# Performance work log

Measured on AMD Instinct MI355X. Metric: run time of the kernel, lower is better.

The kernel has to match this reference:

```python
import jax, jax.numpy as jnp
import numpy as np

B, N, D, K = 4, 8192, 128, 16


def setup_inputs() -> dict:
    key = jax.random.key(0)
    ks = jax.random.split(key, 12)
    w = lambda k, s: (jax.random.normal(k, s, jnp.float32) * 0.02)
    return {
        "xyz": jax.random.normal(ks[0], (B, N, 3), jnp.float32),
        "feat": jax.random.normal(ks[1], (B, N, D), jnp.float32),
        # Linear weights stored as (in, out); apply as x @ W + b
        "Wq": w(ks[2], (D, D)), "bq": jnp.zeros((D,), jnp.float32),
        "Wk": w(ks[3], (D, D)), "bk": jnp.zeros((D,), jnp.float32),
        "Wv": w(ks[4], (D, D)), "bv": jnp.zeros((D,), jnp.float32),
        "Wp1": w(ks[5], (3, D)), "bp1": jnp.zeros((D,), jnp.float32),
        "Wp2": w(ks[6], (D, D)), "bp2": jnp.zeros((D,), jnp.float32),
        "Wo": w(ks[7], (D, D)), "bo": jnp.zeros((D,), jnp.float32),
        "gamma": jnp.float32(0.5),
    }


def reference(xyz, feat, Wq, bq, Wk, bk, Wv, bv, Wp1, bp1, Wp2, bp2, Wo, bo, gamma):
    # pairwise squared distance (B,N,N)
    sq = jnp.sum(xyz * xyz, axis=-1)
    dist = sq[:, :, None] + sq[:, None, :] - 2.0 * jnp.einsum("bnc,bmc->bnm", xyz, xyz)
    # K nearest neighbors (smallest distance)
    _, idx = jax.lax.top_k(-dist, K)  # (B,N,K)
    bidx = jnp.arange(B)[:, None, None]
    n_xyz = xyz[bidx, idx]    # (B,N,K,3)
    n_feat = feat[bidx, idx]  # (B,N,K,D)

    q = (feat @ Wq + bq)[:, :, None, :]    # (B,N,1,D)
    kk = n_feat @ Wk + bk                  # (B,N,K,D)
    v = n_feat @ Wv + bv                   # (B,N,K,D)

    rel_pos = xyz[:, :, None, :] - n_xyz   # (B,N,K,3)
    pos_enc = jax.nn.relu(rel_pos @ Wp1 + bp1) @ Wp2 + bp2  # (B,N,K,D)

    # per-channel-summed attention score, softmax over neighbor axis
    score = jnp.sum(q - kk + pos_enc, axis=-1, keepdims=True)  # (B,N,K,1)
    attn = jax.nn.softmax(score, axis=-2)

    agg = jnp.sum(attn * (v + pos_enc), axis=2)  # (B,N,D)
    out = agg @ Wo + bo
    return feat + gamma * out
```

## Files before the change

kernel.cpp:

```cpp
#include <hip/hip_runtime.h>
#include <hip/hip_bf16.h>

#define BATCH 4
#define NPTS  8192
#define DIM   128
#define KNN   16
#define NROWS (BATCH * NPTS)

#define SPLITS 16
#define RANGE  512
#define TILE   256
#define DEPTH  32
#define DEPTHP 33
#define NSUB   8

using u64  = unsigned long long;
using u32  = unsigned int;

__device__ __forceinline__ unsigned short f2bf(float f) {
    u32 u = __float_as_uint(f);
    u32 r = (u + 0x7FFFu + ((u >> 16) & 1u)) >> 16;
    return (unsigned short)r;
}
__device__ __forceinline__ u32 fordkey(float f) {
    u32 u = __float_as_uint(f);
    return (u & 0x80000000u) ? ~u : (u | 0x80000000u);
}
__device__ __forceinline__ float invkey(u32 k) {
    u32 u = (k & 0x80000000u) ? (k & 0x7FFFFFFFu) : ~k;
    return __uint_as_float(u);
}

__device__ __forceinline__ void insert16u(u32 key, u32* ks) {
    if (key < ks[15]) {
#pragma unroll
        for (int t = 0; t < 16; ++t) {
            u32 lo = key < ks[t] ? key : ks[t];
            u32 hi = key < ks[t] ? ks[t] : key;
            ks[t] = lo;
            key = hi;
        }
    }
}

__device__ __forceinline__ float pdist(float4 me, float4 c) {
    float dot = __fadd_rn(__fadd_rn(__fmul_rn(me.x, c.x), __fmul_rn(me.y, c.y)),
                          __fmul_rn(me.z, c.z));
    return __fsub_rn(__fadd_rn(me.w, c.w), __fmul_rn(2.0f, dot));
}

__global__ __launch_bounds__(256) void prep_weights(const float* __restrict__ Wk,
                                                    const float* __restrict__ Wp2,
                                                    float* __restrict__ wk,
                                                    float* __restrict__ w2) {
    int tid = threadIdx.x;
    int c = tid & 127;
    const float* src = (tid < 128) ? Wk : Wp2;
    float s = 0.f;
    for (int d = 0; d < DIM; ++d) s += src[c * DIM + d];
    if (tid < 128) wk[c] = s;
    else           w2[c] = s;
}

__global__ __launch_bounds__(256) void conv_weights(const float* __restrict__ Wv,
                                                    const float* __restrict__ Wp2,
                                                    const float* __restrict__ Wo,
                                                    u32* __restrict__ Wb) {
    int i = blockIdx.x * 256 + threadIdx.x;
    int which = i >> 13, off = i & 8191;
    const float* W = (which == 0) ? Wv : (which == 1 ? Wp2 : Wo);
    float2 w = ((const float2*)W)[off];
    Wb[i] = (u32)f2bf(w.x) | ((u32)f2bf(w.y) << 16);
}

__global__ __launch_bounds__(256) void prep_points(const float* __restrict__ xyz,
                                                   const float* __restrict__ feat,
                                                   const float* __restrict__ wk,
                                                   float4* __restrict__ pts,
                                                   float* __restrict__ sK) {
    int lid = threadIdx.x & 63;
    int p = blockIdx.x * 4 + (threadIdx.x >> 6);
    float f_lo = feat[(size_t)p * DIM + lid];
    float f_hi = feat[(size_t)p * DIM + 64 + lid];
    float s = fmaf(f_lo, wk[lid], f_hi * wk[64 + lid]);
#pragma unroll
    for (int m = 32; m >= 1; m >>= 1) s += __shfl_xor(s, m);
    if (lid == 0) {
        float x = xyz[p * 3 + 0];
        float y = xyz[p * 3 + 1];
        float z = xyz[p * 3 + 2];
        float sq = __fadd_rn(__fadd_rn(__fmul_rn(x, x), __fmul_rn(y, y)), __fmul_rn(z, z));
        pts[p] = make_float4(x, y, z, sq);
        sK[p] = s;
    }
}

__global__ __launch_bounds__(256) void knn_limpass(const float4* __restrict__ pts,
                                                   float* __restrict__ dlim) {
    __shared__ float4 tile[256];
    int y = blockIdx.y;
    int wavein = threadIdx.x >> 6, lane = threadIdx.x & 63;
    int q = blockIdx.x * 256 + wavein * 64 + lane;
    int b = q >> 13;
    float4 me = pts[q];
    {
        float4 c = pts[b * NPTS + y * 256 + threadIdx.x];
        tile[threadIdx.x] = make_float4(c.x, c.y, c.z, -0.5f * c.w);
    }
    __syncthreads();
    float ks[16];
#pragma unroll
    for (int t = 0; t < 16; ++t) ks[t] = INFINITY;

    for (int jj = 0; jj < 32; ++jj) {
        float4 c = tile[jj];
        float s = fmaf(me.x, c.x, fmaf(me.y, c.y, fmaf(me.z, c.z, c.w)));
        float d = fmaf(-2.0f, s, me.w);
        if (d < ks[15]) {
#pragma unroll
            for (int t = 0; t < 16; ++t) {
                float lo = fminf(d, ks[t]);
                float hi = fmaxf(d, ks[t]);
                ks[t] = lo;
                d = hi;
            }
        }
    }
    float lim = ks[15];
    float A = 0.5f * (me.w - lim);
    for (int c0 = 32; c0 < 256; c0 += 32) {
        u32 mask = 0;
#pragma unroll
        for (int jj = 0; jj < 32; ++jj) {
            float4 c = tile[c0 + jj];
            float s = fmaf(me.x, c.x, fmaf(me.y, c.y, fmaf(me.z, c.z, c.w)));
            mask = (mask << 1) | (u32)(s >= A);
        }
        while (mask) {
            int pos = __builtin_ctz(mask);
            mask &= mask - 1;
            int jj = c0 + 31 - pos;
            float4 c = tile[jj];
            float s = fmaf(me.x, c.x, fmaf(me.y, c.y, fmaf(me.z, c.z, c.w)));
            float d = fmaf(-2.0f, s, me.w);
            if (d < ks[15]) {
#pragma unroll
                for (int t = 0; t < 16; ++t) {
                    float lo = fminf(d, ks[t]);
                    float hi = fmaxf(d, ks[t]);
                    ks[t] = lo;
                    d = hi;
                }
            }
        }
        lim = ks[15];
        A = 0.5f * (me.w - lim);
    }
    dlim[(size_t)y * NROWS + q] = ks[15];
}

__global__ __launch_bounds__(256) void knn_partial(const float4* __restrict__ pts,
                                                   const float* __restrict__ dlim,
                                                   unsigned short* __restrict__ part16) {
    __shared__ float4 tile[TILE];
    __shared__ unsigned char stk[4][64][DEPTHP];
    int r = blockIdx.y;
    int wavein = threadIdx.x >> 6, lane = threadIdx.x & 63;
    int q = blockIdx.x * 256 + wavein * 64 + lane;
    int b = q >> 13;
    float4 me = pts[q];

    float T = dlim[q];
#pragma unroll
    for (int y = 1; y < NSUB; ++y) T = fminf(T, dlim[(size_t)y * NROWS + q]);
    float gate_d = T + 2.0e-4f;
    u32 kk[16];
#pragma unroll
    for (int t = 0; t < 16; ++t) kk[t] = 0xFFFFFFFFu;
    float A = 0.5f * (me.w - gate_d) - 1.0e-4f;
    unsigned char* mystk = stk[wavein][lane];

    for (int tb = 0; tb < RANGE / TILE; ++tb) {
        __syncthreads();
        int jb = r * RANGE + tb * TILE;
        {
            float4 c = pts[b * NPTS + jb + threadIdx.x];
            tile[threadIdx.x] = make_float4(c.x, c.y, c.z, -0.5f * c.w);
        }
        __syncthreads();

        int cnt = 0;
#pragma unroll 4
        for (int jj = 0; jj < TILE; ++jj) {
            float4 c = tile[jj];
            float s = fmaf(me.x, c.x, fmaf(me.y, c.y, fmaf(me.z, c.z, c.w)));
            int slot = cnt < (DEPTH - 1) ? cnt : (DEPTH - 1);
            mystk[slot] = (unsigned char)jj;
            cnt += (s >= A) ? 1 : 0;
        }
        bool over = (cnt >= DEPTH);
        int dn = over ? 0 : cnt;
        for (int i = 0; i < dn; ++i) {
            int jj = mystk[i];
            float4 c = tile[jj];
            float s = fmaf(me.x, c.x, fmaf(me.y, c.y, fmaf(me.z, c.z, c.w)));
            float dt = fmaf(-2.0f, s, me.w);
            u32 key = (fordkey(dt) & 0xFFFFE000u) | (u32)(jb + jj);
            insert16u(key, kk);
        }
        if (__any(over)) {
            if (over) {
                for (int jj = 0; jj < TILE; ++jj) {
                    float4 c = tile[jj];
                    float s = fmaf(me.x, c.x, fmaf(me.y, c.y, fmaf(me.z, c.z, c.w)));
                    if (s >= A) {
                        float dt = fmaf(-2.0f, s, me.w);
                        u32 key = (fordkey(dt) & 0xFFFFE000u) | (u32)(jb + jj);
                        insert16u(key, kk);
                    }
                }
            }
        }
        float nl = invkey((kk[15] & 0xFFFFE000u) | 0x1FFFu) + 1.0e-4f;
        gate_d = (nl < gate_d) ? nl : gate_d;
        A = 0.5f * (me.w - gate_d) - 1.0e-4f;
    }
    u32* dst = (u32*)(part16 + (size_t)q * 256 + r * 16);
#pragma unroll
    for (int t = 0; t < 8; ++t) {
        u32 a = kk[2 * t], c = kk[2 * t + 1];
        u32 i0 = (a == 0xFFFFFFFFu) ? 0xFFFFu : (a & 0x1FFFu);
        u32 i1 = (c == 0xFFFFFFFFu) ? 0xFFFFu : (c & 0x1FFFu);
        dst[t] = i0 | (i1 << 16);
    }
}

__global__ __launch_bounds__(256) void knn_merge(const float4* __restrict__ pts,
                                                 const unsigned short* __restrict__ part16,
                                                 int* __restrict__ idx16) {
    int wavein = threadIdx.x >> 6, lane = threadIdx.x & 63;
    int q = blockIdx.x * 4 + wavein;
    int b = q >> 13;
    float4 me = pts[q];
    ushort4 e = *(const ushort4*)(part16 + (size_t)q * 256 + lane * 4);
    u64 k0, k1, k2, k3;
    {
        u32 id;
        id = e.x; k0 = (id != 0xFFFFu) ? (((u64)fordkey(pdist(me, pts[b * NPTS + id])) << 32) | id) : ~0ull;
        id = e.y; k1 = (id != 0xFFFFu) ? (((u64)fordkey(pdist(me, pts[b * NPTS + id])) << 32) | id) : ~0ull;
        id = e.z; k2 = (id != 0xFFFFu) ? (((u64)fordkey(pdist(me, pts[b * NPTS + id])) << 32) | id) : ~0ull;
        id = e.w; k3 = (id != 0xFFFFu) ? (((u64)fordkey(pdist(me, pts[b * NPTS + id])) << 32) | id) : ~0ull;
    }
    u64 t;
    if (k1 < k0) { t = k0; k0 = k1; k1 = t; }
    if (k3 < k2) { t = k2; k2 = k3; k3 = t; }
    if (k2 < k0) { t = k0; k0 = k2; k2 = t; }
    if (k3 < k1) { t = k1; k1 = k3; k3 = t; }
    if (k2 < k1) { t = k1; k1 = k2; k2 = t; }

    u64 cur = k0;
    int head = 0;
    u64 got = 0;
#pragma unroll
    for (int it = 0; it < 16; ++it) {
        u64 m = cur;
#pragma unroll
        for (int s = 32; s >= 1; s >>= 1) {
            u64 o = __shfl_xor(m, s);
            m = (o < m) ? o : m;
        }
        if (m == cur) {
            head++;
            cur = (head == 1) ? k1 : (head == 2) ? k2 : (head == 3) ? k3 : ~0ull;
        }
        if (lane == it) got = m;
    }
    if (lane < 16) idx16[q * KNN + lane] = (int)(got & 0xFFFFFFFFu);
}

template <int MODE>
__global__ __launch_bounds__(256) void gemm32(const float* __restrict__ X,
                                              const u32* __restrict__ Wb,
                                              const float* __restrict__ bias,
                                              const float* __restrict__ add,
                                              const float* __restrict__ featb,
                                              const float* __restrict__ gammap,
                                              float* __restrict__ outv) {
    __shared__ u32 Ws[DIM * DIM / 2];
    __shared__ float Xs[8 * DIM];
    __shared__ float bs[DIM];
    int tid = threadIdx.x;
    {
        const uint4* src = (const uint4*)Wb;
        uint4* dst = (uint4*)Ws;
        for (int i = tid; i < DIM * DIM / 8; i += 256) dst[i] = src[i];
    }
    if (tid < 128) bs[tid] = bias[tid];
    float gamma = 0.f;
    if (MODE == 2) gamma = *gammap;

    int rowBase = blockIdx.x * 32;
    int d4 = (tid & 31) * 4;
    int row = tid >> 5;

    for (int it = 0; it < 4; ++it) {
        int r0 = rowBase + it * 8;
        __syncthreads();
        ((float4*)Xs)[tid] = ((const float4*)(X + (size_t)r0 * DIM))[tid];
        __syncthreads();

        float a0 = bs[d4], a1 = bs[d4 + 1], a2 = bs[d4 + 2], a3 = bs[d4 + 3];
        const float* xr = &Xs[row * DIM];
#pragma unroll 8
        for (int c = 0; c < DIM; ++c) {
            float x = xr[c];
            uint2 w = *(const uint2*)&Ws[c * (DIM / 2) + (d4 >> 1)];
            a0 = fmaf(x, __uint_as_float(w.x << 16), a0);
            a1 = fmaf(x, __uint_as_float(w.x & 0xFFFF0000u), a1);
            a2 = fmaf(x, __uint_as_float(w.y << 16), a2);
            a3 = fmaf(x, __uint_as_float(w.y & 0xFFFF0000u), a3);
        }
        size_t off = (size_t)(r0 + row) * DIM + d4;
        if (MODE == 1) {
            float4 ad = *(const float4*)(add + off);
            a0 += ad.x; a1 += ad.y; a2 += ad.z; a3 += ad.w;
        }
        if (MODE == 2) {
            float4 fb = *(const float4*)(featb + off);
            a0 = fmaf(gamma, a0, fb.x);
            a1 = fmaf(gamma, a1, fb.y);
            a2 = fmaf(gamma, a2, fb.z);
            a3 = fmaf(gamma, a3, fb.w);
        }
        *(float4*)(outv + off) = make_float4(a0, a1, a2, a3);
    }
}

__global__ __launch_bounds__(256) void stage_c(const float4* __restrict__ pts,
                                               const int* __restrict__ idx16,
                                               const float* __restrict__ sK,
                                               const float* __restrict__ w2,
                                               const float* __restrict__ Wp1,
                                               const float* __restrict__ bp1,
                                               const float* __restrict__ Vf,
                                               float* __restrict__ vagg,
                                               float* __restrict__ hbar) {
    __shared__ float hs[4][KNN * DIM];
    int wavein = threadIdx.x >> 6;
    int lid = threadIdx.x & 63;
    int p = blockIdx.x * 4 + wavein;
    int b = p >> 13;
    float4 me = pts[p];

    float wx_lo = Wp1[lid],        wx_hi = Wp1[64 + lid];
    float wy_lo = Wp1[128 + lid],  wy_hi = Wp1[192 + lid];
    float wz_lo = Wp1[256 + lid],  wz_hi = Wp1[320 + lid];
    float bl    = bp1[lid],        bh    = bp1[64 + lid];
    float w2l   = w2[lid],         w2h   = w2[64 + lid];

    int myidx = idx16[p * KNN + (lid & 15)];
    float* h = hs[wavein];
    float sc = -INFINITY;

    for (int k = 0; k < KNN; ++k) {
        int j = __shfl(myidx, k);
        int g = b * NPTS + j;
        float4 nb = pts[g];
        float rx = me.x - nb.x, ry = me.y - nb.y, rz = me.z - nb.z;
        float h_lo = fmaxf(0.f, fmaf(rx, wx_lo, fmaf(ry, wy_lo, fmaf(rz, wz_lo, bl))));
        float h_hi = fmaxf(0.f, fmaf(rx, wx_hi, fmaf(ry, wy_hi, fmaf(rz, wz_hi, bh))));
        h[k * DIM + lid] = h_lo;
        h[k * DIM + 64 + lid] = h_hi;
        float s = fmaf(h_lo, w2l, h_hi * w2h);
#pragma unroll
        for (int m = 32; m >= 1; m >>= 1) s += __shfl_xor(s, m);
        float score = s - sK[g];
        if (lid == k) sc = score;
    }
    float mx = sc;
#pragma unroll
    for (int m = 8; m >= 1; m >>= 1) mx = fmaxf(mx, __shfl_xor(mx, m));
    float e = (lid < 16) ? __expf(sc - mx) : 0.f;
    float ssum = e;
#pragma unroll
    for (int m = 8; m >= 1; m >>= 1) ssum += __shfl_xor(ssum, m);
    float a = e / ssum;

    float acc_lo = 0.f, acc_hi = 0.f, hb_lo = 0.f, hb_hi = 0.f;
    for (int k = 0; k < KNN; ++k) {
        float ak = __shfl(a, k);
        int j = __shfl(myidx, k);
        size_t g = (size_t)(b * NPTS + j) * DIM;
        acc_lo = fmaf(ak, Vf[g + lid], acc_lo);
        acc_hi = fmaf(ak, Vf[g + 64 + lid], acc_hi);
        hb_lo = fmaf(ak, h[k * DIM + lid], hb_lo);
        hb_hi = fmaf(ak, h[k * DIM + 64 + lid], hb_hi);
    }
    size_t o = (size_t)p * DIM;
    vagg[o + lid] = acc_lo;
    vagg[o + 64 + lid] = acc_hi;
    hbar[o + lid] = hb_lo;
    hbar[o + 64 + lid] = hb_hi;
}

extern "C" void kernel_launch(void* const* d_in, const int* in_sizes, int n_in,
                              void* d_out, int out_size, void* d_ws, size_t ws_size,
                              hipStream_t stream) {
    const float* xyz   = (const float*)d_in[0];
    const float* feat  = (const float*)d_in[1];
    const float* Wk    = (const float*)d_in[4];
    const float* Wv    = (const float*)d_in[6];
    const float* bv    = (const float*)d_in[7];
    const float* Wp1   = (const float*)d_in[8];
    const float* bp1   = (const float*)d_in[9];
    const float* Wp2   = (const float*)d_in[10];
    const float* bp2   = (const float*)d_in[11];
    const float* Wo    = (const float*)d_in[12];
    const float* bo    = (const float*)d_in[13];
    const float* gamma = (const float*)d_in[14];
    float* out = (float*)d_out;

    char* ws = (char*)d_ws;
    const size_t KB = 1024, MB = 1024 * 1024;
    float*  wk    = (float*)(ws + 0);
    float*  w2    = (float*)(ws + 4 * KB);
    float4* pts   = (float4*)(ws + 16 * KB);
    float*  sKv   = (float*)(ws + 544 * KB);
    u32*    Wb    = (u32*)(ws + 688 * KB);
    float*  dlim  = (float*)(ws + 1 * MB);
    unsigned short* part16 = (unsigned short*)(ws + 5 * MB);
    float*  vagg  = (float*)(ws + 5 * MB);
    float*  hbarp = (float*)(ws + 21 * MB);
    int*    idx16 = (int*)(ws + 37 * MB);
    float*  Vf    = (float*)(ws + 39 * MB);
    float*  T1    = (float*)(ws + 39 * MB);

    prep_weights<<<1, 256, 0, stream>>>(Wk, Wp2, wk, w2);
    conv_weights<<<96, 256, 0, stream>>>(Wv, Wp2, Wo, Wb);
    prep_points<<<NROWS / 4, 256, 0, stream>>>(xyz, feat, wk, pts, sKv);
    gemm32<0><<<1024, 256, 0, stream>>>(feat, Wb, bv, nullptr, nullptr, nullptr, Vf);
    knn_limpass<<<dim3(NROWS / 256, NSUB), 256, 0, stream>>>(pts, dlim);
    knn_partial<<<dim3(NROWS / 256, SPLITS), 256, 0, stream>>>(pts, dlim, part16);
    knn_merge<<<NROWS / 4, 256, 0, stream>>>(pts, part16, idx16);
    stage_c<<<NROWS / 4, 256, 0, stream>>>(pts, idx16, sKv, w2, Wp1, bp1, Vf, vagg, hbarp);
    gemm32<1><<<1024, 256, 0, stream>>>(hbarp, Wb + 8192, bp2, vagg, nullptr, nullptr, T1);
    gemm32<2><<<1024, 256, 0, stream>>>(T1, Wb + 16384, bo, nullptr, feat, gamma, out);
}
```

Baseline: 515.8 us.

## Tighten KNN prefilter bound with merged top-16 across windows; bitmask candidate scan

```diff
diff --git a/kernel.cpp b/kernel.cpp
--- a/kernel.cpp
+++ b/kernel.cpp
@@ -10,9 +10,8 @@
 #define SPLITS 16
 #define RANGE  512
 #define TILE   256
-#define DEPTH  32
-#define DEPTHP 33
-#define NSUB   8
+#define LWIN   512
+#define NWIN   4
 
 using u64  = unsigned long long;
 using u32  = unsigned int;
@@ -96,89 +95,116 @@
 }
 
 __global__ __launch_bounds__(256) void knn_limpass(const float4* __restrict__ pts,
-                                                   float* __restrict__ dlim) {
+                                                   float* __restrict__ dl16q) {
     __shared__ float4 tile[256];
     int y = blockIdx.y;
     int wavein = threadIdx.x >> 6, lane = threadIdx.x & 63;
     int q = blockIdx.x * 256 + wavein * 64 + lane;
-    int b = q >> 13;
+    int b = blockIdx.x >> 5;
     float4 me = pts[q];
-    {
-        float4 c = pts[b * NPTS + y * 256 + threadIdx.x];
-        tile[threadIdx.x] = make_float4(c.x, c.y, c.z, -0.5f * c.w);
-    }
-    __syncthreads();
+
     float ks[16];
 #pragma unroll
     for (int t = 0; t < 16; ++t) ks[t] = INFINITY;
-
-    for (int jj = 0; jj < 32; ++jj) {
-        float4 c = tile[jj];
-        float s = fmaf(me.x, c.x, fmaf(me.y, c.y, fmaf(me.z, c.z, c.w)));
-        float d = fmaf(-2.0f, s, me.w);
-        if (d < ks[15]) {
-#pragma unroll
-            for (int t = 0; t < 16; ++t) {
-                float lo = fminf(d, ks[t]);
-                float hi = fmaxf(d, ks[t]);
-                ks[t] = lo;
-                d = hi;
-            }
-        }
-    }
-    float lim = ks[15];
-    float A = 0.5f * (me.w - lim);
-    for (int c0 = 32; c0 < 256; c0 += 32) {
-        u32 mask = 0;
-#pragma unroll
-        for (int jj = 0; jj < 32; ++jj) {
-            float4 c = tile[c0 + jj];
-            float s = fmaf(me.x, c.x, fmaf(me.y, c.y, fmaf(me.z, c.z, c.w)));
-            mask = (mask << 1) | (u32)(s >= A);
-        }
-        while (mask) {
-            int pos = __builtin_ctz(mask);
-            mask &= mask - 1;
-            int jj = c0 + 31 - pos;
-            float4 c = tile[jj];
-            float s = fmaf(me.x, c.x, fmaf(me.y, c.y, fmaf(me.z, c.z, c.w)));
-            float d = fmaf(-2.0f, s, me.w);
-            if (d < ks[15]) {
-#pragma unroll
-                for (int t = 0; t < 16; ++t) {
-                    float lo = fminf(d, ks[t]);
-                    float hi = fmaxf(d, ks[t]);
-                    ks[t] = lo;
-                    d = hi;
+    float lim = INFINITY;
+    float A = -INFINITY;
+
+    for (int tb = 0; tb < LWIN / 256; ++tb) {
+        __syncthreads();
+        {
+            float4 c = pts[b * NPTS + y * LWIN + tb * 256 + threadIdx.x];
+            tile[threadIdx.x] = make_float4(c.x, c.y, c.z, -0.5f * c.w);
+        }
+        __syncthreads();
+
+        int cstart = 0;
+        if (tb == 0) {
+            for (int jj = 0; jj < 32; ++jj) {
+                float4 c = tile[jj];
+                float s = fmaf(me.x, c.x, fmaf(me.y, c.y, fmaf(me.z, c.z, c.w)));
+                float d = fmaf(-2.0f, s, me.w);
+                if (d < ks[15]) {
+#pragma unroll
+                    for (int t = 0; t < 16; ++t) {
+                        float lo = fminf(d, ks[t]);
+                        float hi = fmaxf(d, ks[t]);
+                        ks[t] = lo;
+                        d = hi;
+                    }
                 }
             }
-        }
-        lim = ks[15];
-        A = 0.5f * (me.w - lim);
-    }
-    dlim[(size_t)y * NROWS + q] = ks[15];
+            lim = ks[15];
+            A = 0.5f * (me.w - lim);
+            cstart = 32;
+        }
+        for (int c0 = cstart; c0 < 256; c0 += 32) {
+            u32 mask = 0;
+#pragma unroll
+            for (int jj = 0; jj < 32; ++jj) {
+                float4 c = tile[c0 + jj];
+                float s = fmaf(me.x, c.x, fmaf(me.y, c.y, fmaf(me.z, c.z, c.w)));
+                mask = (mask << 1) | (u32)(s >= A);
+            }
+            while (mask) {
+                int pos = __builtin_ctz(mask);
+                mask &= mask - 1;
+                int jj = c0 + 31 - pos;
+                float4 c = tile[jj];
+                float s = fmaf(me.x, c.x, fmaf(me.y, c.y, fmaf(me.z, c.z, c.w)));
+                float d = fmaf(-2.0f, s, me.w);
+                if (d < ks[15]) {
+#pragma unroll
+                    for (int t = 0; t < 16; ++t) {
+                        float lo = fminf(d, ks[t]);
+                        float hi = fmaxf(d, ks[t]);
+                        ks[t] = lo;
+                        d = hi;
+                    }
+                }
+            }
+            lim = ks[15];
+            A = 0.5f * (me.w - lim);
+        }
+    }
+    float4* dst = (float4*)(dl16q + (size_t)q * 64 + y * 16);
+    dst[0] = make_float4(ks[0], ks[1], ks[2], ks[3]);
+    dst[1] = make_float4(ks[4], ks[5], ks[6], ks[7]);
+    dst[2] = make_float4(ks[8], ks[9], ks[10], ks[11]);
+    dst[3] = make_float4(ks[12], ks[13], ks[14], ks[15]);
+}
+
+__global__ __launch_bounds__(256) void bound_merge(const float* __restrict__ dl16q,
+                                                   float* __restrict__ Tq) {
+    int wavein = threadIdx.x >> 6, lane = threadIdx.x & 63;
+    int q = blockIdx.x * 4 + wavein;
+    float v = dl16q[(size_t)q * 64 + lane];
+    float got = v;
+#pragma unroll
+    for (int it = 0; it < 16; ++it) {
+        float m = v;
+#pragma unroll
+        for (int s = 32; s >= 1; s >>= 1) m = fminf(m, __shfl_xor(m, s));
+        if (v == m) v = INFINITY;
+        got = m;
+    }
+    if (lane == 0) Tq[q] = got;
 }
 
 __global__ __launch_bounds__(256) void knn_partial(const float4* __restrict__ pts,
-                                                   const float* __restrict__ dlim,
+                                                   const float* __restrict__ Tq,
                                                    unsigned short* __restrict__ part16) {
     __shared__ float4 tile[TILE];
-    __shared__ unsigned char stk[4][64][DEPTHP];
     int r = blockIdx.y;
     int wavein = threadIdx.x >> 6, lane = threadIdx.x & 63;
     int q = blockIdx.x * 256 + wavein * 64 + lane;
     int b = q >> 13;
     float4 me = pts[q];
 
-    float T = dlim[q];
-#pragma unroll
-    for (int y = 1; y < NSUB; ++y) T = fminf(T, dlim[(size_t)y * NROWS + q]);
-    float gate_d = T + 2.0e-4f;
+    float gate_d = Tq[q] + 2.0e-4f;
     u32 kk[16];
 #pragma unroll
     for (int t = 0; t < 16; ++t) kk[t] = 0xFFFFFFFFu;
     float A = 0.5f * (me.w - gate_d) - 1.0e-4f;
-    unsigned char* mystk = stk[wavein][lane];
 
     for (int tb = 0; tb < RANGE / TILE; ++tb) {
         __syncthreads();
@@ -189,37 +215,37 @@
         }
         __syncthreads();
 
-        int cnt = 0;
-#pragma unroll 4
-        for (int jj = 0; jj < TILE; ++jj) {
-            float4 c = tile[jj];
-            float s = fmaf(me.x, c.x, fmaf(me.y, c.y, fmaf(me.z, c.z, c.w)));
-            int slot = cnt < (DEPTH - 1) ? cnt : (DEPTH - 1);
-            mystk[slot] = (unsigned char)jj;
-            cnt += (s >= A) ? 1 : 0;
-        }
-        bool over = (cnt >= DEPTH);
-        int dn = over ? 0 : cnt;
-        for (int i = 0; i < dn; ++i) {
-            int jj = mystk[i];
+        u32 m[8];
+#pragma unroll
+        for (int w = 0; w < 8; ++w) {
+            u32 mask = 0;
+#pragma unroll
+            for (int jj = 0; jj < 32; ++jj) {
+                float4 c = tile[w * 32 + jj];
+                float s = fmaf(me.x, c.x, fmaf(me.y, c.y, fmaf(me.z, c.z, c.w)));
+                mask = (mask << 1) | (u32)(s >= A);
+            }
+            m[w] = mask;
+        }
+        int cnt = __popc(m[0]) + __popc(m[1]) + __popc(m[2]) + __popc(m[3]) +
+                  __popc(m[4]) + __popc(m[5]) + __popc(m[6]) + __popc(m[7]);
+
+        u32 cur = m[0];
+        int w = 0;
+        for (int i = 0; i < cnt; ++i) {
+            while (cur == 0) {
+                ++w;
+                cur = (w == 1) ? m[1] : (w == 2) ? m[2] : (w == 3) ? m[3] :
+                      (w == 4) ? m[4] : (w == 5) ? m[5] : (w == 6) ? m[6] : m[7];
+            }
+            int pos = __builtin_ctz(cur);
+            cur &= cur - 1;
+            int jj = (w << 5) + (31 - pos);
             float4 c = tile[jj];
             float s = fmaf(me.x, c.x, fmaf(me.y, c.y, fmaf(me.z, c.z, c.w)));
             float dt = fmaf(-2.0f, s, me.w);
             u32 key = (fordkey(dt) & 0xFFFFE000u) | (u32)(jb + jj);
             insert16u(key, kk);
-        }
-        if (__any(over)) {
-            if (over) {
-                for (int jj = 0; jj < TILE; ++jj) {
-                    float4 c = tile[jj];
-                    float s = fmaf(me.x, c.x, fmaf(me.y, c.y, fmaf(me.z, c.z, c.w)));
-                    if (s >= A) {
-                        float dt = fmaf(-2.0f, s, me.w);
-                        u32 key = (fordkey(dt) & 0xFFFFE000u) | (u32)(jb + jj);
-                        insert16u(key, kk);
-                    }
-                }
-            }
         }
         float nl = invkey((kk[15] & 0xFFFFE000u) | 0x1FFFu) + 1.0e-4f;
         gate_d = (nl < gate_d) ? nl : gate_d;
@@ -427,7 +453,8 @@
     float4* pts   = (float4*)(ws + 16 * KB);
     float*  sKv   = (float*)(ws + 544 * KB);
     u32*    Wb    = (u32*)(ws + 688 * KB);
-    float*  dlim  = (float*)(ws + 1 * MB);
+    float*  Tq    = (float*)(ws + 1 * MB);
+    float*  dl16q = (float*)(ws + 5 * MB);
     unsigned short* part16 = (unsigned short*)(ws + 5 * MB);
     float*  vagg  = (float*)(ws + 5 * MB);
     float*  hbarp = (float*)(ws + 21 * MB);
@@ -439,8 +466,9 @@
     conv_weights<<<96, 256, 0, stream>>>(Wv, Wp2, Wo, Wb);
     prep_points<<<NROWS / 4, 256, 0, stream>>>(xyz, feat, wk, pts, sKv);
     gemm32<0><<<1024, 256, 0, stream>>>(feat, Wb, bv, nullptr, nullptr, nullptr, Vf);
-    knn_limpass<<<dim3(NROWS / 256, NSUB), 256, 0, stream>>>(pts, dlim);
-    knn_partial<<<dim3(NROWS / 256, SPLITS), 256, 0, stream>>>(pts, dlim, part16);
+    knn_limpass<<<dim3(NROWS / 256, NWIN), 256, 0, stream>>>(pts, dl16q);
+    bound_merge<<<NROWS / 4, 256, 0, stream>>>(dl16q, Tq);
+    knn_partial<<<dim3(NROWS / 256, SPLITS), 256, 0, stream>>>(pts, Tq, part16);
     knn_merge<<<NROWS / 4, 256, 0, stream>>>(pts, part16, idx16);
     stage_c<<<NROWS / 4, 256, 0, stream>>>(pts, idx16, sKv, w2, Wp1, bp1, Vf, vagg, hbarp);
     gemm32<1><<<1024, 256, 0, stream>>>(hbarp, Wb + 8192, bp2, vagg, nullptr, nullptr, T1);
```

Result: no change. 523.9 us (+1.6%).
